# Optimization experiments

Hardware: AMD Instinct MI355X
Metric: run time of the kernel (lower is better)

The kernel has to match this reference:

```python
import jax, jax.numpy as jnp
import numpy as np

NCODEBOOKS, K, SUBVEC = 32, 16, 128
IN_F, OUT_F = 4096, 2048
BATCH, SEQ = 2, 1024


def setup_inputs() -> dict:
    key = jax.random.key(0)
    k1, k2, k3, k4, k5 = jax.random.split(key, 5)
    return {
        "x": jax.random.normal(k1, (BATCH, SEQ, IN_F), dtype=jnp.float32),
        "centroids": jax.random.normal(k2, (NCODEBOOKS, K, SUBVEC), dtype=jnp.float32),
        "weight": jax.random.normal(k3, (NCODEBOOKS, SUBVEC, OUT_F), dtype=jnp.float32),
        "inverse_temperature_logit": jax.random.normal(k4, (1,), dtype=jnp.float32),
        "bias": jax.random.normal(k5, (OUT_F,), dtype=jnp.float32),
    }


def reference(x, centroids, weight, inverse_temperature_logit, bias):
    shape = x.shape[:-1]
    C, k, d = centroids.shape
    # [N, C, d] -> [C, N, d]
    xr = jnp.transpose(x.reshape(-1, C, d), (1, 0, 2))
    # Euclidean cdist per codebook: [C, N, k]
    x2 = jnp.sum(xr * xr, axis=-1)[:, :, None]
    c2 = jnp.sum(centroids * centroids, axis=-1)[:, None, :]
    xc = jnp.einsum('cnd,ckd->cnk', xr, centroids)
    dist = jnp.sqrt(jnp.maximum(x2 + c2 - 2.0 * xc, 0.0))
    inv_temp = jax.nn.softplus(inverse_temperature_logit) + 1.0  # [1]
    attention = jax.nn.softmax(-dist * inv_temp, axis=-1)  # [C, N, k]
    lut = jnp.einsum('ckd,cdo->cko', centroids, weight)  # [C, k, O]
    training_output = jnp.einsum('cnk,cko->no', attention, lut)  # [N, O]
    # one-hot argmin matmul == direct gather of lut rows
    idx = jnp.argmin(dist, axis=-1)  # [C, N]
    gathered = jnp.take_along_axis(lut, idx[:, :, None], axis=1)  # [C, N, O]
    inference_output = jnp.sum(gathered, axis=0)  # [N, O]
    # straight-through estimator
    output = training_output - jax.lax.stop_gradient(training_output - inference_output)
    output = output + bias
    return output.reshape(*shape, lut.shape[-1])
```

## Files before the change

### kernel.cpp

```cpp
#include <hip/hip_runtime.h>

#define NCB 32
#define KK 16
#define DD 128
#define IN_F 4096
#define OUT_F 2048
#define NTOK 2048

#define LUT_BLOCKS 128
#define TT 32
#define IDX_BLOCKS ((NTOK / TT) * NCB)

__global__ __launch_bounds__(256, 4) void fused_lut_idx(
    const float* __restrict__ centroids, const float* __restrict__ weight,
    const float* __restrict__ x, const float* __restrict__ bias,
    float* __restrict__ lut, unsigned char* __restrict__ idxb) {
    const int tid = threadIdx.x;

    if (blockIdx.x < LUT_BLOCKS) {
        const int c  = blockIdx.x >> 2;
        const int kh = (blockIdx.x >> 1) & 1;
        const int oh = blockIdx.x & 1;
        const int o  = oh * 1024 + tid * 4;
        const float* cb = centroids + ((size_t)c * KK + kh * 8) * DD;
        const float* wb = weight + (size_t)c * DD * OUT_F + o;
        float4 acc[8];
#pragma unroll
        for (int k = 0; k < 8; ++k) acc[k] = make_float4(0.f, 0.f, 0.f, 0.f);
#pragma unroll 2
        for (int d4 = 0; d4 < DD / 4; ++d4) {
            float4 w0 = *(const float4*)(wb + (size_t)(d4 * 4 + 0) * OUT_F);
            float4 w1 = *(const float4*)(wb + (size_t)(d4 * 4 + 1) * OUT_F);
            float4 w2 = *(const float4*)(wb + (size_t)(d4 * 4 + 2) * OUT_F);
            float4 w3 = *(const float4*)(wb + (size_t)(d4 * 4 + 3) * OUT_F);
#pragma unroll
            for (int k = 0; k < 8; ++k) {
                float4 cv = *(const float4*)(cb + k * DD + d4 * 4);
                acc[k].x += cv.x * w0.x + cv.y * w1.x + cv.z * w2.x + cv.w * w3.x;
                acc[k].y += cv.x * w0.y + cv.y * w1.y + cv.z * w2.y + cv.w * w3.y;
                acc[k].z += cv.x * w0.z + cv.y * w1.z + cv.z * w2.z + cv.w * w3.z;
                acc[k].w += cv.x * w0.w + cv.y * w1.w + cv.z * w2.w + cv.w * w3.w;
            }
        }
        if (c == 0) {
            float4 bv = *(const float4*)(bias + o);
#pragma unroll
            for (int k = 0; k < 8; ++k) {
                acc[k].x += bv.x; acc[k].y += bv.y;
                acc[k].z += bv.z; acc[k].w += bv.w;
            }
        }
#pragma unroll
        for (int k = 0; k < 8; ++k)
            *(float4*)(lut + ((size_t)c * KK + kh * 8 + k) * OUT_F + o) = acc[k];
    } else {
        const int bid = blockIdx.x - LUT_BLOCKS;
        const int c = bid & (NCB - 1);
        const int t0 = (bid >> 5) * TT;
        const int th_q = tid & 3;
        const int th_k = (tid >> 2) & 3;
        const int th_t = tid >> 4;

        const float* xg = x + (size_t)(t0 + th_t * 2) * IN_F + c * DD + th_q * 32;
        const float* cg = centroids + ((size_t)c * KK + th_k * 4) * DD + th_q * 32;

        float acc[2][4], sq[4];
#pragma unroll
        for (int r = 0; r < 2; ++r)
#pragma unroll
            for (int kk = 0; kk < 4; ++kk) acc[r][kk] = 0.f;
#pragma unroll
        for (int kk = 0; kk < 4; ++kk) sq[kk] = 0.f;

#pragma unroll
        for (int chunk = 0; chunk < 8; ++chunk) {
            float4 ca[4];
#pragma unroll
            for (int kk = 0; kk < 4; ++kk)
                ca[kk] = *(const float4*)(cg + kk * DD + chunk * 4);
#pragma unroll
            for (int kk = 0; kk < 4; ++kk)
                sq[kk] += ca[kk].x * ca[kk].x + ca[kk].y * ca[kk].y
                        + ca[kk].z * ca[kk].z + ca[kk].w * ca[kk].w;
#pragma unroll
            for (int r = 0; r < 2; ++r) {
                float4 xr = *(const float4*)(xg + (size_t)r * IN_F + chunk * 4);
#pragma unroll
                for (int kk = 0; kk < 4; ++kk)
                    acc[r][kk] += xr.x * ca[kk].x + xr.y * ca[kk].y
                                + xr.z * ca[kk].z + xr.w * ca[kk].w;
            }
        }
#pragma unroll
        for (int kk = 0; kk < 4; ++kk) {
            float a = sq[kk];
            a += __shfl_xor(a, 1);
            a += __shfl_xor(a, 2);
            sq[kk] = a;
        }
#pragma unroll
        for (int r = 0; r < 2; ++r)
#pragma unroll
            for (int kk = 0; kk < 4; ++kk) {
                float a = acc[r][kk];
                a += __shfl_xor(a, 1);
                a += __shfl_xor(a, 2);
                acc[r][kk] = a;
            }
#pragma unroll
        for (int r = 0; r < 2; ++r) {
            float best = sq[0] - 2.f * acc[r][0];
            int bi = th_k * 4;
#pragma unroll
            for (int kk = 1; kk < 4; ++kk) {
                float v = sq[kk] - 2.f * acc[r][kk];
                if (v < best) { best = v; bi = th_k * 4 + kk; }
            }
#pragma unroll
            for (int s = 4; s <= 8; s <<= 1) {
                float ov = __shfl_xor(best, s);
                int oi = __shfl_xor(bi, s);
                if (ov < best || (ov == best && oi < bi)) { best = ov; bi = oi; }
            }
            if ((tid & 15) == 0)
                idxb[(size_t)(t0 + th_t * 2 + r) * NCB + c] = (unsigned char)bi;
        }
    }
}

__global__ __launch_bounds__(256) void gather_kernel(const float* __restrict__ lut,
                                                     const unsigned char* __restrict__ idxb,
                                                     float* __restrict__ out) {
    const int o0 = blockIdx.x * 32;
    const int t0 = blockIdx.y * 64;
    const int og = threadIdx.x & 7;
    const int tl = threadIdx.x >> 3;
    const int o = o0 + og * 4;

    const int ta = t0 + tl;
    const int tb = ta + 32;
    const uint4 ivA0 = *(const uint4*)(idxb + (size_t)ta * NCB);
    const uint4 ivA1 = *(const uint4*)(idxb + (size_t)ta * NCB + 16);
    const uint4 ivB0 = *(const uint4*)(idxb + (size_t)tb * NCB);
    const uint4 ivB1 = *(const uint4*)(idxb + (size_t)tb * NCB + 16);
    unsigned int uA[8] = {ivA0.x, ivA0.y, ivA0.z, ivA0.w, ivA1.x, ivA1.y, ivA1.z, ivA1.w};
    unsigned int uB[8] = {ivB0.x, ivB0.y, ivB0.z, ivB0.w, ivB1.x, ivB1.y, ivB1.z, ivB1.w};

    float4 accA = make_float4(0.f, 0.f, 0.f, 0.f);
    float4 accB = make_float4(0.f, 0.f, 0.f, 0.f);
#pragma unroll
    for (int c4 = 0; c4 < 8; ++c4) {
        unsigned int uvA = uA[c4], uvB = uB[c4];
#pragma unroll
        for (int b = 0; b < 4; ++b) {
            int cc = c4 * 4 + b;
            int kA = (uvA >> (8 * b)) & 0xff;
            int kB = (uvB >> (8 * b)) & 0xff;
            const float4 vA = *(const float4*)(lut + (size_t)(cc * KK + kA) * OUT_F + o);
            const float4 vB = *(const float4*)(lut + (size_t)(cc * KK + kB) * OUT_F + o);
            accA.x += vA.x; accA.y += vA.y; accA.z += vA.z; accA.w += vA.w;
            accB.x += vB.x; accB.y += vB.y; accB.z += vB.z; accB.w += vB.w;
        }
    }
    *(float4*)(out + (size_t)ta * OUT_F + o) = accA;
    *(float4*)(out + (size_t)tb * OUT_F + o) = accB;
}

extern "C" void kernel_launch(void* const* d_in, const int* in_sizes, int n_in,
                              void* d_out, int out_size, void* d_ws, size_t ws_size,
                              hipStream_t stream) {
    const float* x         = (const float*)d_in[0];
    const float* centroids = (const float*)d_in[1];
    const float* weight    = (const float*)d_in[2];
    const float* bias      = (const float*)d_in[4];
    float* out = (float*)d_out;

    float* lut = (float*)d_ws;
    unsigned char* idxb = (unsigned char*)d_ws + (4u << 20);

    fused_lut_idx<<<LUT_BLOCKS + IDX_BLOCKS, 256, 0, stream>>>(
        centroids, weight, x, bias, lut, idxb);
    gather_kernel<<<dim3(OUT_F / 32, NTOK / 64), 256, 0, stream>>>(lut, idxb, out);
}
```

Baseline: 172.2 us.

## Stage x and centroid tiles in LDS for idx blocks; split LUT work finer

The index-computation blocks now load their 32-token x tile and the codebook's centroids into padded shared memory with coalesced float4 loads, then read operands from LDS instead of issuing strided global loads per thread. The padding strides are chosen to reduce bank conflicts. Separately, the LUT part is split across twice as many blocks, each computing 4 centroids by 256 outputs with a scalar-d inner loop, to raise parallelism. The cost is about 28KB of static shared memory per block, which applies to the LUT blocks too and may limit occupancy, plus a barrier.

```diff
diff --git a/kernel.cpp b/kernel.cpp
--- a/kernel.cpp
+++ b/kernel.cpp
@@ -7,52 +7,54 @@
 #define OUT_F 2048
 #define NTOK 2048
 
-#define LUT_BLOCKS 128
+#define LUT_BLOCKS 256
 #define TT 32
 #define IDX_BLOCKS ((NTOK / TT) * NCB)
+
+#define XS_STRIDE 148
+#define CS_OFF (TT * XS_STRIDE)
+#define SMEM_FLOATS (CS_OFF + KK * 164)
 
 __global__ __launch_bounds__(256, 4) void fused_lut_idx(
     const float* __restrict__ centroids, const float* __restrict__ weight,
     const float* __restrict__ x, const float* __restrict__ bias,
     float* __restrict__ lut, unsigned char* __restrict__ idxb) {
+    __shared__ float smem[SMEM_FLOATS];
     const int tid = threadIdx.x;
 
     if (blockIdx.x < LUT_BLOCKS) {
-        const int c  = blockIdx.x >> 2;
-        const int kh = (blockIdx.x >> 1) & 1;
-        const int oh = blockIdx.x & 1;
-        const int o  = oh * 1024 + tid * 4;
-        const float* cb = centroids + ((size_t)c * KK + kh * 8) * DD;
+        const int c  = blockIdx.x >> 3;
+        const int ot = blockIdx.x & 7;
+        const int kq = tid >> 6;
+        const int o  = ot * 256 + (tid & 63) * 4;
+        const float* cb = centroids + ((size_t)c * KK + kq * 4) * DD;
         const float* wb = weight + (size_t)c * DD * OUT_F + o;
-        float4 acc[8];
-#pragma unroll
-        for (int k = 0; k < 8; ++k) acc[k] = make_float4(0.f, 0.f, 0.f, 0.f);
-#pragma unroll 2
-        for (int d4 = 0; d4 < DD / 4; ++d4) {
-            float4 w0 = *(const float4*)(wb + (size_t)(d4 * 4 + 0) * OUT_F);
-            float4 w1 = *(const float4*)(wb + (size_t)(d4 * 4 + 1) * OUT_F);
-            float4 w2 = *(const float4*)(wb + (size_t)(d4 * 4 + 2) * OUT_F);
-            float4 w3 = *(const float4*)(wb + (size_t)(d4 * 4 + 3) * OUT_F);
-#pragma unroll
-            for (int k = 0; k < 8; ++k) {
-                float4 cv = *(const float4*)(cb + k * DD + d4 * 4);
-                acc[k].x += cv.x * w0.x + cv.y * w1.x + cv.z * w2.x + cv.w * w3.x;
-                acc[k].y += cv.x * w0.y + cv.y * w1.y + cv.z * w2.y + cv.w * w3.y;
-                acc[k].z += cv.x * w0.z + cv.y * w1.z + cv.z * w2.z + cv.w * w3.z;
-                acc[k].w += cv.x * w0.w + cv.y * w1.w + cv.z * w2.w + cv.w * w3.w;
+        float4 acc[4];
+#pragma unroll
+        for (int k = 0; k < 4; ++k) acc[k] = make_float4(0.f, 0.f, 0.f, 0.f);
+#pragma unroll 4
+        for (int d = 0; d < DD; ++d) {
+            float4 w = *(const float4*)(wb + (size_t)d * OUT_F);
+#pragma unroll
+            for (int k = 0; k < 4; ++k) {
+                float cv = cb[k * DD + d];
+                acc[k].x += cv * w.x;
+                acc[k].y += cv * w.y;
+                acc[k].z += cv * w.z;
+                acc[k].w += cv * w.w;
             }
         }
         if (c == 0) {
             float4 bv = *(const float4*)(bias + o);
 #pragma unroll
-            for (int k = 0; k < 8; ++k) {
+            for (int k = 0; k < 4; ++k) {
                 acc[k].x += bv.x; acc[k].y += bv.y;
                 acc[k].z += bv.z; acc[k].w += bv.w;
             }
         }
 #pragma unroll
-        for (int k = 0; k < 8; ++k)
-            *(float4*)(lut + ((size_t)c * KK + kh * 8 + k) * OUT_F + o) = acc[k];
+        for (int k = 0; k < 4; ++k)
+            *(float4*)(lut + ((size_t)c * KK + kq * 4 + k) * OUT_F + o) = acc[k];
     } else {
         const int bid = blockIdx.x - LUT_BLOCKS;
         const int c = bid & (NCB - 1);
@@ -60,9 +62,27 @@
         const int th_q = tid & 3;
         const int th_k = (tid >> 2) & 3;
         const int th_t = tid >> 4;
-
-        const float* xg = x + (size_t)(t0 + th_t * 2) * IN_F + c * DD + th_q * 32;
-        const float* cg = centroids + ((size_t)c * KK + th_k * 4) * DD + th_q * 32;
+        float* xs = smem;
+        float* cs = smem + CS_OFF;
+
+        {
+            const float* xg = x + (size_t)t0 * IN_F + c * DD;
+#pragma unroll
+            for (int i = 0; i < (TT * DD / 4) / 256; ++i) {
+                int p = i * 256 + tid;
+                int t = p >> 5, f4 = p & 31;
+                int q = f4 >> 3, jj = f4 & 7;
+                float4 v = *(const float4*)(xg + (size_t)t * IN_F + f4 * 4);
+                *(float4*)(xs + t * XS_STRIDE + q * 36 + jj * 4) = v;
+            }
+        }
+        for (int p = tid; p < KK * 32; p += 256) {
+            int k = p >> 5, f4 = p & 31;
+            int q = f4 >> 3, jj = f4 & 7;
+            *(float4*)(cs + k * 164 + q * 40 + jj * 4) =
+                *(const float4*)(centroids + ((size_t)c * KK + k) * DD + f4 * 4);
+        }
+        __syncthreads();
 
         float acc[2][4], sq[4];
 #pragma unroll
@@ -77,14 +97,15 @@
             float4 ca[4];
 #pragma unroll
             for (int kk = 0; kk < 4; ++kk)
-                ca[kk] = *(const float4*)(cg + kk * DD + chunk * 4);
+                ca[kk] = *(const float4*)(cs + (th_k * 4 + kk) * 164 + th_q * 40 + chunk * 4);
 #pragma unroll
             for (int kk = 0; kk < 4; ++kk)
                 sq[kk] += ca[kk].x * ca[kk].x + ca[kk].y * ca[kk].y
                         + ca[kk].z * ca[kk].z + ca[kk].w * ca[kk].w;
 #pragma unroll
             for (int r = 0; r < 2; ++r) {
-                float4 xr = *(const float4*)(xg + (size_t)r * IN_F + chunk * 4);
+                float4 xr = *(const float4*)(xs + (th_t * 2 + r) * XS_STRIDE
+                                             + th_q * 36 + chunk * 4);
 #pragma unroll
                 for (int kk = 0; kk < 4; ++kk)
                     acc[r][kk] += xr.x * ca[kk].x + xr.y * ca[kk].y
```

Measured after the change: 161.9 us. 1.06x faster.

## Split fused LUT/index kernel, stage x and centroids in LDS, widen LUT grid

Applied to the files above, without the earlier changes.

Splits the fused kernel into a separate index kernel and LUT kernel. The index kernel now loads its x and centroid tiles into padded shared memory with coalesced float4 loads before the distance computation, in place of strided per-thread global reads. The LUT kernel uses 512 blocks, each thread computing 2 centroid rows instead of 8, to spread the weight-streaming work across more CUs. The cost is an extra kernel launch and the loss of overlap between the two phases.

```diff
diff --git a/kernel.cpp b/kernel.cpp
--- a/kernel.cpp
+++ b/kernel.cpp
@@ -7,125 +7,161 @@
 #define OUT_F 2048
 #define NTOK 2048
 
-#define LUT_BLOCKS 128
 #define TT 32
 #define IDX_BLOCKS ((NTOK / TT) * NCB)
 
-__global__ __launch_bounds__(256, 4) void fused_lut_idx(
-    const float* __restrict__ centroids, const float* __restrict__ weight,
-    const float* __restrict__ x, const float* __restrict__ bias,
-    float* __restrict__ lut, unsigned char* __restrict__ idxb) {
+#define XS_STRIDE 148
+#define CS_OFF (TT * XS_STRIDE)
+#define SMEM_FLOATS (CS_OFF + KK * 164)
+
+__global__ __launch_bounds__(256, 4) void idx_kernel(
+    const float* __restrict__ centroids, const float* __restrict__ x,
+    unsigned char* __restrict__ idxb) {
+    __shared__ float smem[SMEM_FLOATS];
     const int tid = threadIdx.x;
-
-    if (blockIdx.x < LUT_BLOCKS) {
-        const int c  = blockIdx.x >> 2;
-        const int kh = (blockIdx.x >> 1) & 1;
-        const int oh = blockIdx.x & 1;
-        const int o  = oh * 1024 + tid * 4;
-        const float* cb = centroids + ((size_t)c * KK + kh * 8) * DD;
-        const float* wb = weight + (size_t)c * DD * OUT_F + o;
-        float4 acc[8];
-#pragma unroll
-        for (int k = 0; k < 8; ++k) acc[k] = make_float4(0.f, 0.f, 0.f, 0.f);
-#pragma unroll 2
-        for (int d4 = 0; d4 < DD / 4; ++d4) {
-            float4 w0 = *(const float4*)(wb + (size_t)(d4 * 4 + 0) * OUT_F);
-            float4 w1 = *(const float4*)(wb + (size_t)(d4 * 4 + 1) * OUT_F);
-            float4 w2 = *(const float4*)(wb + (size_t)(d4 * 4 + 2) * OUT_F);
-            float4 w3 = *(const float4*)(wb + (size_t)(d4 * 4 + 3) * OUT_F);
-#pragma unroll
-            for (int k = 0; k < 8; ++k) {
-                float4 cv = *(const float4*)(cb + k * DD + d4 * 4);
-                acc[k].x += cv.x * w0.x + cv.y * w1.x + cv.z * w2.x + cv.w * w3.x;
-                acc[k].y += cv.x * w0.y + cv.y * w1.y + cv.z * w2.y + cv.w * w3.y;
-                acc[k].z += cv.x * w0.z + cv.y * w1.z + cv.z * w2.z + cv.w * w3.z;
-                acc[k].w += cv.x * w0.w + cv.y * w1.w + cv.z * w2.w + cv.w * w3.w;
-            }
-        }
-        if (c == 0) {
-            float4 bv = *(const float4*)(bias + o);
-#pragma unroll
-            for (int k = 0; k < 8; ++k) {
-                acc[k].x += bv.x; acc[k].y += bv.y;
-                acc[k].z += bv.z; acc[k].w += bv.w;
-            }
-        }
-#pragma unroll
-        for (int k = 0; k < 8; ++k)
-            *(float4*)(lut + ((size_t)c * KK + kh * 8 + k) * OUT_F + o) = acc[k];
-    } else {
-        const int bid = blockIdx.x - LUT_BLOCKS;
-        const int c = bid & (NCB - 1);
-        const int t0 = (bid >> 5) * TT;
-        const int th_q = tid & 3;
-        const int th_k = (tid >> 2) & 3;
-        const int th_t = tid >> 4;
-
-        const float* xg = x + (size_t)(t0 + th_t * 2) * IN_F + c * DD + th_q * 32;
-        const float* cg = centroids + ((size_t)c * KK + th_k * 4) * DD + th_q * 32;
-
-        float acc[2][4], sq[4];
-#pragma unroll
-        for (int r = 0; r < 2; ++r)
-#pragma unroll
-            for (int kk = 0; kk < 4; ++kk) acc[r][kk] = 0.f;
-#pragma unroll
-        for (int kk = 0; kk < 4; ++kk) sq[kk] = 0.f;
-
-#pragma unroll
-        for (int chunk = 0; chunk < 8; ++chunk) {
-            float4 ca[4];
+    const int c = blockIdx.x & (NCB - 1);
+    const int t0 = (blockIdx.x >> 5) * TT;
+    const int th_q = tid & 3;
+    const int th_k = (tid >> 2) & 3;
+    const int th_t = tid >> 4;
+    float* xs = smem;
+    float* cs = smem + CS_OFF;
+
+    float4 xv[4], cv[2];
+    int xt[4], xq[4], xj[4], ck[2], cq[2], cj[2];
+    {
+        const float* xg = x + (size_t)t0 * IN_F + c * DD;
+#pragma unroll
+        for (int i = 0; i < 4; ++i) {
+            int p = i * 256 + tid;
+            xt[i] = p >> 5;
+            int f4 = p & 31;
+            xq[i] = f4 >> 3; xj[i] = f4 & 7;
+            xv[i] = *(const float4*)(xg + (size_t)xt[i] * IN_F + f4 * 4);
+        }
+#pragma unroll
+        for (int i = 0; i < 2; ++i) {
+            int p = i * 256 + tid;
+            ck[i] = p >> 5;
+            int f4 = p & 31;
+            cq[i] = f4 >> 3; cj[i] = f4 & 7;
+            cv[i] = *(const float4*)(centroids + ((size_t)c * KK + ck[i]) * DD + f4 * 4);
+        }
+#pragma unroll
+        for (int i = 0; i < 4; ++i)
+            *(float4*)(xs + xt[i] * XS_STRIDE + xq[i] * 36 + xj[i] * 4) = xv[i];
+#pragma unroll
+        for (int i = 0; i < 2; ++i)
+            *(float4*)(cs + ck[i] * 164 + cq[i] * 40 + cj[i] * 4) = cv[i];
+    }
+    __syncthreads();
+
+    float acc[2][4], sq[4];
+#pragma unroll
+    for (int r = 0; r < 2; ++r)
+#pragma unroll
+        for (int kk = 0; kk < 4; ++kk) acc[r][kk] = 0.f;
+#pragma unroll
+    for (int kk = 0; kk < 4; ++kk) sq[kk] = 0.f;
+
+#pragma unroll
+    for (int chunk = 0; chunk < 8; ++chunk) {
+        float4 ca[4];
+#pragma unroll
+        for (int kk = 0; kk < 4; ++kk)
+            ca[kk] = *(const float4*)(cs + (th_k * 4 + kk) * 164 + th_q * 40 + chunk * 4);
+#pragma unroll
+        for (int kk = 0; kk < 4; ++kk)
+            sq[kk] += ca[kk].x * ca[kk].x + ca[kk].y * ca[kk].y
+                    + ca[kk].z * ca[kk].z + ca[kk].w * ca[kk].w;
+#pragma unroll
+        for (int r = 0; r < 2; ++r) {
+            float4 xr = *(const float4*)(xs + (th_t * 2 + r) * XS_STRIDE
+                                         + th_q * 36 + chunk * 4);
 #pragma unroll
             for (int kk = 0; kk < 4; ++kk)
-                ca[kk] = *(const float4*)(cg + kk * DD + chunk * 4);
-#pragma unroll
-            for (int kk = 0; kk < 4; ++kk)
-                sq[kk] += ca[kk].x * ca[kk].x + ca[kk].y * ca[kk].y
-                        + ca[kk].z * ca[kk].z + ca[kk].w * ca[kk].w;
-#pragma unroll
-            for (int r = 0; r < 2; ++r) {
-                float4 xr = *(const float4*)(xg + (size_t)r * IN_F + chunk * 4);
-#pragma unroll
-                for (int kk = 0; kk < 4; ++kk)
-                    acc[r][kk] += xr.x * ca[kk].x + xr.y * ca[kk].y
-                                + xr.z * ca[kk].z + xr.w * ca[kk].w;
-            }
-        }
+                acc[r][kk] += xr.x * ca[kk].x + xr.y * ca[kk].y
+                            + xr.z * ca[kk].z + xr.w * ca[kk].w;
+        }
+    }
+#pragma unroll
+    for (int kk = 0; kk < 4; ++kk) {
+        float a = sq[kk];
+        a += __shfl_xor(a, 1);
+        a += __shfl_xor(a, 2);
+        sq[kk] = a;
+    }
+#pragma unroll
+    for (int r = 0; r < 2; ++r)
 #pragma unroll
         for (int kk = 0; kk < 4; ++kk) {
-            float a = sq[kk];
+            float a = acc[r][kk];
             a += __shfl_xor(a, 1);
             a += __shfl_xor(a, 2);
-            sq[kk] = a;
-        }
-#pragma unroll
-        for (int r = 0; r < 2; ++r)
-#pragma unroll
-            for (int kk = 0; kk < 4; ++kk) {
-                float a = acc[r][kk];
-                a += __shfl_xor(a, 1);
-                a += __shfl_xor(a, 2);
-                acc[r][kk] = a;
-            }
-#pragma unroll
-        for (int r = 0; r < 2; ++r) {
-            float best = sq[0] - 2.f * acc[r][0];
-            int bi = th_k * 4;
-#pragma unroll
-            for (int kk = 1; kk < 4; ++kk) {
-                float v = sq[kk] - 2.f * acc[r][kk];
-                if (v < best) { best = v; bi = th_k * 4 + kk; }
-            }
-#pragma unroll
-            for (int s = 4; s <= 8; s <<= 1) {
-                float ov = __shfl_xor(best, s);
-                int oi = __shfl_xor(bi, s);
-                if (ov < best || (ov == best && oi < bi)) { best = ov; bi = oi; }
-            }
-            if ((tid & 15) == 0)
-                idxb[(size_t)(t0 + th_t * 2 + r) * NCB + c] = (unsigned char)bi;
-        }
-    }
+            acc[r][kk] = a;
+        }
+#pragma unroll
+    for (int r = 0; r < 2; ++r) {
+        float best = sq[0] - 2.f * acc[r][0];
+        int bi = th_k * 4;
+#pragma unroll
+        for (int kk = 1; kk < 4; ++kk) {
+            float v = sq[kk] - 2.f * acc[r][kk];
+            if (v < best) { best = v; bi = th_k * 4 + kk; }
+        }
+#pragma unroll
+        for (int s = 4; s <= 8; s <<= 1) {
+            float ov = __shfl_xor(best, s);
+            int oi = __shfl_xor(bi, s);
+            if (ov < best || (ov == best && oi < bi)) { best = ov; bi = oi; }
+        }
+        if ((tid & 15) == 0)
+            idxb[(size_t)(t0 + th_t * 2 + r) * NCB + c] = (unsigned char)bi;
+    }
+}
+
+#define LUT_BLOCKS 512
+__global__ __launch_bounds__(256, 4) void lut_kernel(
+    const float* __restrict__ centroids, const float* __restrict__ weight,
+    const float* __restrict__ bias, float* __restrict__ lut) {
+    const int tid = threadIdx.x;
+    const int c  = blockIdx.x >> 4;
+    const int kh = (blockIdx.x >> 3) & 1;
+    const int oq = blockIdx.x & 7;
+    const int kq = __builtin_amdgcn_readfirstlane(tid >> 6);
+    const int k0 = kh * 8 + kq * 2;
+    const int o  = oq * 256 + (tid & 63) * 4;
+    const float* cb = centroids + ((size_t)c * KK + k0) * DD;
+    const float* wb = weight + (size_t)c * DD * OUT_F + o;
+    float4 acc[2];
+#pragma unroll
+    for (int k = 0; k < 2; ++k) acc[k] = make_float4(0.f, 0.f, 0.f, 0.f);
+#pragma unroll 2
+    for (int d4 = 0; d4 < DD / 4; ++d4) {
+        float4 w0 = *(const float4*)(wb + (size_t)(d4 * 4 + 0) * OUT_F);
+        float4 w1 = *(const float4*)(wb + (size_t)(d4 * 4 + 1) * OUT_F);
+        float4 w2 = *(const float4*)(wb + (size_t)(d4 * 4 + 2) * OUT_F);
+        float4 w3 = *(const float4*)(wb + (size_t)(d4 * 4 + 3) * OUT_F);
+#pragma unroll
+        for (int k = 0; k < 2; ++k) {
+            float4 cv = *(const float4*)(cb + k * DD + d4 * 4);
+            acc[k].x += cv.x * w0.x + cv.y * w1.x + cv.z * w2.x + cv.w * w3.x;
+            acc[k].y += cv.x * w0.y + cv.y * w1.y + cv.z * w2.y + cv.w * w3.y;
+            acc[k].z += cv.x * w0.z + cv.y * w1.z + cv.z * w2.z + cv.w * w3.z;
+            acc[k].w += cv.x * w0.w + cv.y * w1.w + cv.z * w2.w + cv.w * w3.w;
+        }
+    }
+    if (c == 0) {
+        float4 bv = *(const float4*)(bias + o);
+#pragma unroll
+        for (int k = 0; k < 2; ++k) {
+            acc[k].x += bv.x; acc[k].y += bv.y;
+            acc[k].z += bv.z; acc[k].w += bv.w;
+        }
+    }
+#pragma unroll
+    for (int k = 0; k < 2; ++k)
+        *(float4*)(lut + ((size_t)c * KK + k0 + k) * OUT_F + o) = acc[k];
 }
 
 __global__ __launch_bounds__(256) void gather_kernel(const float* __restrict__ lut,
@@ -178,7 +214,7 @@
     float* lut = (float*)d_ws;
     unsigned char* idxb = (unsigned char*)d_ws + (4u << 20);
 
-    fused_lut_idx<<<LUT_BLOCKS + IDX_BLOCKS, 256, 0, stream>>>(
-        centroids, weight, x, bias, lut, idxb);
+    idx_kernel<<<IDX_BLOCKS, 256, 0, stream>>>(centroids, x, idxb);
+    lut_kernel<<<LUT_BLOCKS, 256, 0, stream>>>(centroids, weight, bias, lut);
     gather_kernel<<<dim3(OUT_F / 32, NTOK / 64), 256, 0, stream>>>(lut, idxb, out);
 }
```

Result: faster. 162.7 us (-5.5%).
